# Kernel tuning notes

Hardware: AMD Instinct MI355X
Metric: run time of the kernel (lower is better)

Reference implementation:

```python
import jax, jax.numpy as jnp
import numpy as np

N_NODES = 100000
N_EDGES = 1250000
D_IN = 64
D_OUT = 64


def setup_inputs() -> dict:
    key = jax.random.key(0)
    k1, k2, k3, k4, k5 = jax.random.split(key, 5)
    x = jax.random.normal(k1, (N_NODES, D_IN), dtype=jnp.float32)
    edge_index = jax.random.randint(k2, (2, N_EDGES), 0, N_NODES, dtype=jnp.int64)
    # Linear weights stored torch-style as [out, in]
    w_neigh = jax.random.normal(k3, (D_OUT, D_IN), dtype=jnp.float32) / np.sqrt(D_IN)
    w_self = jax.random.normal(k4, (D_OUT, D_IN), dtype=jnp.float32) / np.sqrt(D_IN)
    b_self = jax.random.normal(k5, (D_OUT,), dtype=jnp.float32) * 0.01
    return {"x": x, "edge_index": edge_index, "w_neigh": w_neigh, "w_self": w_self, "b_self": b_self}


def reference(x, edge_index, w_neigh, w_self, b_self):
    num_nodes = x.shape[0]
    src, dst = edge_index[0], edge_index[1]
    # mean aggregation of neighbor features: scatter-add then divide by in-degree
    agg = jax.ops.segment_sum(x[src], dst, num_segments=num_nodes)  # [N, d]
    degree = jax.ops.segment_sum(jnp.ones_like(dst, dtype=x.dtype), dst, num_segments=num_nodes)
    degree = jnp.maximum(degree, 1.0)
    agg = agg / degree[:, None]
    return agg @ w_neigh.T + x @ w_self.T + b_self
```

## Files before the change

### kernel.cpp

```cpp
#include <hip/hip_runtime.h>

#define N_NODES 100000
#define N_EDGES 1250000
#define D 64
#define BSH 6
#define BNODES 64
#define NB 1563
#define WSW 68
#define G 512
#define CHUNK 2444
#define BIN_BLOCKS 128
#define BIN_CHUNK ((N_EDGES + BIN_BLOCKS - 1) / BIN_BLOCKS)

typedef unsigned int u32;
typedef short bf16x8 __attribute__((ext_vector_type(8)));
typedef float f32x4 __attribute__((ext_vector_type(4)));

__device__ __forceinline__ u32 pack_bf16(float lo, float hi) {
    u32 a = __float_as_uint(lo);
    u32 b = __float_as_uint(hi);
    a = (a + 0x7fffu + ((a >> 16) & 1u)) >> 16;
    b = (b + 0x7fffu + ((b >> 16) & 1u)) >> 16;
    return a | (b << 16);
}

__global__ void __launch_bounds__(256) k_wprep2(const float* __restrict__ wn,
                                                const float* __restrict__ wsf,
                                                u32* __restrict__ bfrag) {
    int i = blockIdx.x * 256 + threadIdx.x;
    if (i >= 4096) return;
    int t = i >> 9, h = (i >> 8) & 1, l = (i >> 2) & 63, q = i & 3;
    int k0 = h * 32 + (l >> 4) * 8 + 2 * q;
    int n = t * 16 + (l & 15);
    const float* w = (n < 64) ? &wn[(size_t)n * 64] : &wsf[(size_t)(n - 64) * 64];
    bfrag[i] = pack_bf16(w[k0], w[k0 + 1]);
}

__global__ void __launch_bounds__(256) k_hist(const int* __restrict__ ei,
                                              u32* __restrict__ ghist) {
    __shared__ u32 hist[NB];
    int tid = threadIdx.x;
    int g = blockIdx.x;
    int e0 = g * CHUNK, e1 = min(e0 + CHUNK, N_EDGES);
    for (int i = tid; i < NB; i += 256) hist[i] = 0;
    __syncthreads();
    const int4* dp = (const int4*)(ei + N_EDGES + e0);
    int nv = (e1 - e0) >> 2;
    for (int i = tid; i < nv; i += 256) {
        int4 d4 = dp[i];
        atomicAdd(&hist[d4.x >> BSH], 1u);
        atomicAdd(&hist[d4.y >> BSH], 1u);
        atomicAdd(&hist[d4.z >> BSH], 1u);
        atomicAdd(&hist[d4.w >> BSH], 1u);
    }
    __syncthreads();
    for (int i = tid; i < NB; i += 256)
        ghist[(size_t)i * G + g] = hist[i];
}

__global__ void __launch_bounds__(512) k_scanB(const u32* __restrict__ ghist,
                                               u32* __restrict__ gbase,
                                               u32* __restrict__ bcnt) {
    __shared__ u32 wt[8];
    int t = threadIdx.x;
    int b = blockIdx.x;
    int lane = t & 63, wv = t >> 6;
    u32 v = ghist[(size_t)b * G + t];
    u32 s = v;
#pragma unroll
    for (int off = 1; off < 64; off <<= 1) {
        u32 n = __shfl_up(s, off, 64);
        if (lane >= off) s += n;
    }
    if (lane == 63) wt[wv] = s;
    __syncthreads();
    u32 add = 0;
#pragma unroll
    for (int q = 0; q < 8; ++q) add += (q < wv) ? wt[q] : 0u;
    u32 incl = s + add;
    gbase[(size_t)b * G + t] = incl - v;
    if (t == G - 1) bcnt[b] = incl;
}

__global__ void __launch_bounds__(256) k_scat(const int* __restrict__ ei,
                                              const u32* __restrict__ gbase,
                                              u32* __restrict__ binned,
                                              int cap) {
    __shared__ u32 cur[NB];
    int tid = threadIdx.x;
    int g = blockIdx.x;
    int e0 = g * CHUNK, e1 = min(e0 + CHUNK, N_EDGES);
    for (int i = tid; i < NB; i += 256)
        cur[i] = gbase[(size_t)i * G + g];
    __syncthreads();
    const int4* sp = (const int4*)(ei + e0);
    const int4* dp = (const int4*)(ei + N_EDGES + e0);
    int nv = (e1 - e0) >> 2;
    for (int i = tid; i < nv; i += 256) {
        int4 s4 = sp[i];
        int4 d4 = dp[i];
        int ss[4] = {s4.x, s4.y, s4.z, s4.w};
        int dd[4] = {d4.x, d4.y, d4.z, d4.w};
#pragma unroll
        for (int u = 0; u < 4; ++u) {
            int b = dd[u] >> BSH;
            u32 loc = atomicAdd(&cur[b], 1u);
            if (loc < (u32)cap)
                binned[(size_t)b * cap + loc] = ((u32)ss[u] << BSH) | (u32)(dd[u] & (BNODES - 1));
        }
    }
}

__global__ void __launch_bounds__(256) k_mm(const float* __restrict__ x,
                                            const u32* __restrict__ bfrag,
                                            const float* __restrict__ bias,
                                            u32* __restrict__ y16,
                                            float* __restrict__ zout) {
    int tid = threadIdx.x;
    int w = tid >> 6, l = tid & 63;
    int lg = l >> 4, c = l & 15;
    int nodebase = blockIdx.x * 128 + w * 32;

    union FU { uint4 u; bf16x8 v; };

    bf16x8 af[2][2];
#pragma unroll
    for (int m = 0; m < 2; ++m) {
        int node = nodebase + m * 16 + c;
        if (node >= N_NODES) node = N_NODES - 1;
        const float4* xr = (const float4*)(x + (size_t)node * D);
#pragma unroll
        for (int h = 0; h < 2; ++h) {
            float4 p0 = xr[h * 8 + lg * 2];
            float4 p1 = xr[h * 8 + lg * 2 + 1];
            FU au;
            au.u.x = pack_bf16(p0.x, p0.y);
            au.u.y = pack_bf16(p0.z, p0.w);
            au.u.z = pack_bf16(p1.x, p1.y);
            au.u.w = pack_bf16(p1.z, p1.w);
            af[m][h] = au.v;
        }
    }

    f32x4 acc[2][8];
#pragma unroll
    for (int m = 0; m < 2; ++m) {
#pragma unroll
        for (int t = 0; t < 4; ++t) acc[m][t] = (f32x4){0.f, 0.f, 0.f, 0.f};
#pragma unroll
        for (int t = 4; t < 8; ++t) {
            float bb = bias[(t - 4) * 16 + c];
            acc[m][t] = (f32x4){bb, bb, bb, bb};
        }
    }

    const uint4* bp = (const uint4*)bfrag;
#pragma unroll
    for (int tc = 0; tc < 2; ++tc) {
        bf16x8 bf[4][2];
#pragma unroll
        for (int tt = 0; tt < 4; ++tt)
#pragma unroll
            for (int h = 0; h < 2; ++h) {
                FU bu;
                bu.u = bp[(((tc * 4 + tt) * 2 + h) * 64) + l];
                bf[tt][h] = bu.v;
            }
#pragma unroll
        for (int m = 0; m < 2; ++m)
#pragma unroll
            for (int tt = 0; tt < 4; ++tt) {
                int t = tc * 4 + tt;
                acc[m][t] = __builtin_amdgcn_mfma_f32_16x16x32_bf16(
                    af[m][0], bf[tt][0], acc[m][t], 0, 0, 0);
                acc[m][t] = __builtin_amdgcn_mfma_f32_16x16x32_bf16(
                    af[m][1], bf[tt][1], acc[m][t], 0, 0, 0);
            }
    }

#pragma unroll
    for (int m = 0; m < 2; ++m) {
        int rowbase = nodebase + m * 16 + lg * 4;
#pragma unroll
        for (int r = 0; r < 4; ++r) {
            int node = rowbase + r;
            bool ok = node < N_NODES;
#pragma unroll
            for (int t = 4; t < 8; ++t) {
                if (ok) zout[(size_t)node * D + (t - 4) * 16 + c] = acc[m][t][r];
            }
#pragma unroll
            for (int t = 0; t < 4; ++t) {
                float v = acc[m][t][r];
                float o = __shfl_xor(v, 1);
                if (ok && !(c & 1))
                    y16[(size_t)node * 32 + t * 8 + (c >> 1)] = pack_bf16(v, o);
            }
        }
    }
}

__global__ void __launch_bounds__(256) k_sort(u32* __restrict__ binned,
                                              const u32* __restrict__ bcnt,
                                              int cap,
                                              uint2* __restrict__ meta) {
    __shared__ u32 eh[1024];
    __shared__ u32 hist[BNODES];
    __shared__ u32 cur[BNODES];
    int tid = threadIdx.x;
    int b = blockIdx.x;
    int cnt = min((int)bcnt[b], cap);
    u32* seg = binned + (size_t)b * cap;

    if (tid < BNODES) hist[tid] = 0;
    __syncthreads();
    const uint4* segv = (const uint4*)seg;
    int nv = cnt >> 2;
    for (int i = tid; i < nv; i += 256) {
        uint4 w4 = segv[i];
        *(uint4*)&eh[4 * i] = w4;
        atomicAdd(&hist[w4.x & (BNODES - 1)], 1u);
        atomicAdd(&hist[w4.y & (BNODES - 1)], 1u);
        atomicAdd(&hist[w4.z & (BNODES - 1)], 1u);
        atomicAdd(&hist[w4.w & (BNODES - 1)], 1u);
    }
    for (int i = (cnt & ~3) + tid; i < cnt; i += 256) {
        u32 w = seg[i];
        eh[i] = w;
        atomicAdd(&hist[w & (BNODES - 1)], 1u);
    }
    __syncthreads();
    if (tid < BNODES) {
        u32 v = hist[tid];
        u32 s = v;
#pragma unroll
        for (int off = 1; off < 64; off <<= 1) {
            u32 n = __shfl_up(s, off, 64);
            if (tid >= off) s += n;
        }
        u32 excl = s - v;
        cur[tid] = excl;
        int node = (b << BSH) + tid;
        if (node < N_NODES)
            meta[node] = make_uint2((u32)((size_t)b * cap + excl), v);
    }
    __syncthreads();
    for (int i = tid; i < cnt; i += 256) {
        u32 w = eh[i];
        u32 p = atomicAdd(&cur[w & (BNODES - 1)], 1u);
        seg[p] = w >> BSH;
    }
}

__global__ void __launch_bounds__(256) k_gather_yz(const u32* __restrict__ y16,
                                                   const u32* __restrict__ binned,
                                                   const uint2* __restrict__ meta,
                                                   float* __restrict__ io) {
    int tid = blockIdx.x * 256 + threadIdx.x;
    int node = tid >> 6;
    if (node >= N_NODES) return;
    int lane = threadIdx.x & 63;
    int sub = lane >> 4;
    int pr = lane & 15;
    const uint2* yv = (const uint2*)y16;
    uint2 m = meta[node];
    u32 o0 = m.x, dg = m.y;

    u32 myidx = 0;
    if (lane < (int)dg) myidx = binned[o0 + lane];

    float a0 = 0.f, a1 = 0.f, a2 = 0.f, a3 = 0.f;
    u32 dmain = min(dg, 64u);
    for (u32 r = 0; r < dmain; r += 32) {
        uint2 w[8];
#pragma unroll
        for (int t = 0; t < 8; ++t) {
            u32 e = r + 4 * t + sub;
            u32 idx = (u32)__shfl((int)myidx, (int)(e & 63));
            w[t] = make_uint2(0u, 0u);
            if (e < dmain) w[t] = yv[(size_t)idx * 16 + pr];
        }
#pragma unroll
        for (int t = 0; t < 8; ++t) {
            if (r + 4u * (u32)t < dmain) {
                a0 += __uint_as_float(w[t].x << 16);
                a1 += __uint_as_float(w[t].x & 0xffff0000u);
                a2 += __uint_as_float(w[t].y << 16);
                a3 += __uint_as_float(w[t].y & 0xffff0000u);
            }
        }
    }
    for (u32 j = o0 + 64; j < o0 + dg; j += 16) {
#pragma unroll
        for (int t = 0; t < 4; ++t) {
            u32 ie = j + 4 * t + sub;
            if (ie < o0 + dg) {
                u32 idx = binned[ie];
                uint2 w = yv[(size_t)idx * 16 + pr];
                a0 += __uint_as_float(w.x << 16);
                a1 += __uint_as_float(w.x & 0xffff0000u);
                a2 += __uint_as_float(w.y << 16);
                a3 += __uint_as_float(w.y & 0xffff0000u);
            }
        }
    }

    a0 += __shfl_xor(a0, 16); a1 += __shfl_xor(a1, 16);
    a2 += __shfl_xor(a2, 16); a3 += __shfl_xor(a3, 16);
    a0 += __shfl_xor(a0, 32); a1 += __shfl_xor(a1, 32);
    a2 += __shfl_xor(a2, 32); a3 += __shfl_xor(a3, 32);
    if (sub == 0) {
        float inv = 1.0f / (float)max(dg, 1u);
        float4 z = *(const float4*)&io[(size_t)node * D + 4 * pr];
        *(float4*)&io[(size_t)node * D + 4 * pr] =
            make_float4(z.x + a0 * inv, z.y + a1 * inv, z.z + a2 * inv, z.w + a3 * inv);
    }
}

__global__ void __launch_bounds__(256) k_bin2(const int* __restrict__ ei,
                                              u32* __restrict__ bcnt,
                                              u32* __restrict__ binned,
                                              int cap) {
    __shared__ u32 hist[NB];
    __shared__ u32 rbase[NB];
    int tid = threadIdx.x;
    int e0 = blockIdx.x * BIN_CHUNK;
    int e1 = min(e0 + BIN_CHUNK, N_EDGES);
    const int* dstp = ei + N_EDGES;
    for (int i = tid; i < NB; i += 256) hist[i] = 0;
    __syncthreads();
    for (int e = e0 + tid; e < e1; e += 256)
        atomicAdd(&hist[dstp[e] >> BSH], 1u);
    __syncthreads();
    for (int i = tid; i < NB; i += 256) {
        u32 h = hist[i];
        rbase[i] = h ? atomicAdd(&bcnt[i], h) : 0u;
        hist[i] = 0;
    }
    __syncthreads();
    for (int e = e0 + tid; e < e1; e += 256) {
        int d = dstp[e];
        int s = ei[e];
        int b = d >> BSH;
        u32 loc = atomicAdd(&hist[b], 1u);
        u32 slot = rbase[b] + loc;
        if (slot < (u32)cap)
            binned[(size_t)b * cap + slot] = ((u32)s << BSH) | (u32)(d & (BNODES - 1));
    }
}

__global__ void __launch_bounds__(256) k_sort_fb(u32* __restrict__ binned,
                                                 const u32* __restrict__ bcnt,
                                                 int cap,
                                                 u32* __restrict__ offs,
                                                 u32* __restrict__ deg) {
    __shared__ u32 eh[1024];
    __shared__ u32 hist[BNODES];
    __shared__ u32 cur[BNODES];
    int tid = threadIdx.x;
    int b = blockIdx.x;
    int cnt = min((int)bcnt[b], cap);
    u32* seg = binned + (size_t)b * cap;
    if (tid < BNODES) hist[tid] = 0;
    __syncthreads();
    for (int i = tid; i < cnt; i += 256) {
        u32 w = seg[i];
        eh[i] = w;
        atomicAdd(&hist[w & (BNODES - 1)], 1u);
    }
    __syncthreads();
    if (tid < BNODES) {
        u32 v = hist[tid];
        u32 s = v;
#pragma unroll
        for (int off = 1; off < 64; off <<= 1) {
            u32 n = __shfl_up(s, off, 64);
            if (tid >= off) s += n;
        }
        u32 excl = s - v;
        cur[tid] = excl;
        int node = (b << BSH) + tid;
        if (node < N_NODES) {
            offs[node] = (u32)((size_t)b * cap + excl);
            deg[node] = v;
        }
    }
    __syncthreads();
    for (int i = tid; i < cnt; i += 256) {
        u32 w = eh[i];
        u32 p = atomicAdd(&cur[w & (BNODES - 1)], 1u);
        seg[p] = w >> BSH;
    }
}

__global__ void __launch_bounds__(256) k_gather32(const float* __restrict__ x,
                                                  const u32* __restrict__ binned,
                                                  const u32* __restrict__ offs,
                                                  const u32* __restrict__ deg,
                                                  float* __restrict__ agg) {
    int tid = blockIdx.x * 256 + threadIdx.x;
    int node = tid >> 6;
    int d = tid & 63;
    if (node >= N_NODES) return;
    u32 o0 = offs[node], dg = deg[node];
    u32 o1 = o0 + dg;
    float s = 0.f;
    u32 j = o0;
    for (; j + 8 <= o1; j += 8) {
        u32 e[8];
        float v[8];
#pragma unroll
        for (int t = 0; t < 8; ++t) e[t] = binned[j + t];
#pragma unroll
        for (int t = 0; t < 8; ++t) v[t] = x[(size_t)e[t] * D + d];
#pragma unroll
        for (int t = 0; t < 8; ++t) s += v[t];
    }
    for (; j < o1; ++j) s += x[(size_t)binned[j] * D + d];
    agg[(size_t)node * D + d] = s / (float)max(dg, 1u);
}

__global__ void __launch_bounds__(256) k_gemm_fb(const float* __restrict__ x,
                                                 const float* __restrict__ wn,
                                                 const float* __restrict__ wsf,
                                                 const float* __restrict__ bias,
                                                 float* __restrict__ io) {
    __shared__ float At[BNODES * WSW];
    __shared__ float Wt[128 * WSW];
    int tid = threadIdx.x;
    int base = blockIdx.x * 64;
    const float4* iop = (const float4*)io;
    const float4* xp  = (const float4*)x;
    for (int i = tid; i < 4096; i += 256) {
        int d = i >> 6, k = i & 63;
        Wt[k * WSW + d] = wn[i];
        Wt[(64 + k) * WSW + d] = wsf[i];
    }
    for (int i = tid; i < 1024; i += 256) {
        int r = i >> 4, q = i & 15;
        int node = base + r;
        float4 v = make_float4(0.f, 0.f, 0.f, 0.f);
        if (node < N_NODES) v = iop[(size_t)node * 16 + q];
        *(float4*)&At[r * WSW + q * 4] = v;
    }
    __syncthreads();
    int tn = tid >> 4, td = tid & 15;
    int n0 = tn * 4, d0 = td * 4;
    float4 b4 = *(const float4*)&bias[d0];
    float acc[4][4];
#pragma unroll
    for (int i = 0; i < 4; ++i) {
        acc[i][0] = b4.x; acc[i][1] = b4.y; acc[i][2] = b4.z; acc[i][3] = b4.w;
    }
#pragma unroll 8
    for (int kc = 0; kc < 16; ++kc) {
        float4 a[4], w[4];
#pragma unroll
        for (int i = 0; i < 4; ++i) a[i] = *(const float4*)&At[(n0 + i) * WSW + kc * 4];
#pragma unroll
        for (int t = 0; t < 4; ++t) w[t] = *(const float4*)&Wt[(kc * 4 + t) * WSW + d0];
#pragma unroll
        for (int i = 0; i < 4; ++i) {
            const float av[4] = {a[i].x, a[i].y, a[i].z, a[i].w};
#pragma unroll
            for (int t = 0; t < 4; ++t) {
                acc[i][0] += av[t] * w[t].x; acc[i][1] += av[t] * w[t].y;
                acc[i][2] += av[t] * w[t].z; acc[i][3] += av[t] * w[t].w;
            }
        }
    }
    __syncthreads();
    for (int i = tid; i < 1024; i += 256) {
        int r = i >> 4, q = i & 15;
        int node = base + r;
        float4 v = make_float4(0.f, 0.f, 0.f, 0.f);
        if (node < N_NODES) v = xp[(size_t)node * 16 + q];
        *(float4*)&At[r * WSW + q * 4] = v;
    }
    __syncthreads();
#pragma unroll 8
    for (int kc = 0; kc < 16; ++kc) {
        float4 a[4], w[4];
#pragma unroll
        for (int i = 0; i < 4; ++i) a[i] = *(const float4*)&At[(n0 + i) * WSW + kc * 4];
#pragma unroll
        for (int t = 0; t < 4; ++t) w[t] = *(const float4*)&Wt[(64 + kc * 4 + t) * WSW + d0];
#pragma unroll
        for (int i = 0; i < 4; ++i) {
            const float av[4] = {a[i].x, a[i].y, a[i].z, a[i].w};
#pragma unroll
            for (int t = 0; t < 4; ++t) {
                acc[i][0] += av[t] * w[t].x; acc[i][1] += av[t] * w[t].y;
                acc[i][2] += av[t] * w[t].z; acc[i][3] += av[t] * w[t].w;
            }
        }
    }
#pragma unroll
    for (int i = 0; i < 4; ++i) {
        int node = base + n0 + i;
        if (node < N_NODES) {
            *(float4*)&io[(size_t)node * D + d0] =
                make_float4(acc[i][0], acc[i][1], acc[i][2], acc[i][3]);
        }
    }
}

extern "C" void kernel_launch(void* const* d_in, const int* in_sizes, int n_in,
                              void* d_out, int out_size, void* d_ws, size_t ws_size,
                              hipStream_t stream) {
    const float* x = (const float*)d_in[0];
    const int* ei = (const int*)d_in[1];
    const float* wn = (const float*)d_in[2];
    const float* wsf = (const float*)d_in[3];
    const float* bias = (const float*)d_in[4];
    float* out = (float*)d_out;

    u32* metaw = (u32*)d_ws;
    u32* bcnt = metaw + 2 * N_NODES;
    u32* bfrag = bcnt + ((NB + 15) & ~15);
    u32* y16 = bfrag + 8192;
    const size_t Y16W = (size_t)N_NODES * (D / 2);
    u32* binned = y16 + Y16W;
    size_t fixed = 2 * (size_t)N_NODES + ((NB + 15) & ~15) + 8192;

    if (ws_size / 4 >= fixed + Y16W + (size_t)NB * 1024) {
        const int cap = 1024;
        u32* ghist = binned;
        u32* gbase = y16;
        k_wprep2<<<16, 256, 0, stream>>>(wn, wsf, bfrag);
        k_hist<<<G, 256, 0, stream>>>(ei, ghist);
        k_scanB<<<NB, 512, 0, stream>>>(ghist, gbase, bcnt);
        k_scat<<<G, 256, 0, stream>>>(ei, gbase, binned, cap);
        k_mm<<<(N_NODES + 127) / 128, 256, 0, stream>>>(x, bfrag, bias, y16, out);
        k_sort<<<NB, 256, 0, stream>>>(binned, bcnt, cap, (uint2*)metaw);
        k_gather_yz<<<(N_NODES * 64) / 256, 256, 0, stream>>>(y16, binned, (const uint2*)metaw, out);
    } else {
        u32* offs = metaw;
        u32* deg = offs + N_NODES;
        binned = bfrag;
        size_t avail = ws_size / 4 - (fixed - 8192);
        size_t capz = (avail / NB) & ~(size_t)3;
        int cap = (int)(capz < 1024 ? capz : 1024);
        hipMemsetAsync(bcnt, 0, ((NB + 15) & ~15) * sizeof(u32), stream);
        k_bin2<<<BIN_BLOCKS, 256, 0, stream>>>(ei, bcnt, binned, cap);
        k_sort_fb<<<NB, 256, 0, stream>>>(binned, bcnt, cap, offs, deg);
        k_gather32<<<(N_NODES * 64) / 256, 256, 0, stream>>>(x, binned, offs, deg, out);
        k_gemm_fb<<<(N_NODES + 63) / 64, 256, 0, stream>>>(x, wn, wsf, bias, out);
    }
}
```

Baseline: 100.3 us.

## Fuse weight prep into histogram and matmul into scatter kernel

Merges the weight-fragment prep kernel into the histogram kernel as an extra block, and merges the dense bf16 matmul into the edge scatter kernel via blockIdx dispatch. This cuts two kernel launches and lets the compute-bound matmul blocks run alongside the atomic-heavy scatter blocks. To avoid aliasing, ghist and gbase move to dedicated workspace regions, which raises the workspace requirement for the fast path. The merged kernel's LDS and register footprint is the maximum of the two roles, which may lower occupancy for the matmul blocks.

```diff
diff --git a/kernel.cpp b/kernel.cpp
--- a/kernel.cpp
+++ b/kernel.cpp
@@ -9,6 +9,7 @@
 #define WSW 68
 #define G 512
 #define CHUNK 2444
+#define MM_BLOCKS ((N_NODES + 127) / 128)
 #define BIN_BLOCKS 128
 #define BIN_CHUNK ((N_EDGES + BIN_BLOCKS - 1) / BIN_BLOCKS)
 
@@ -24,38 +25,39 @@
     return a | (b << 16);
 }
 
-__global__ void __launch_bounds__(256) k_wprep2(const float* __restrict__ wn,
-                                                const float* __restrict__ wsf,
-                                                u32* __restrict__ bfrag) {
-    int i = blockIdx.x * 256 + threadIdx.x;
-    if (i >= 4096) return;
-    int t = i >> 9, h = (i >> 8) & 1, l = (i >> 2) & 63, q = i & 3;
-    int k0 = h * 32 + (l >> 4) * 8 + 2 * q;
-    int n = t * 16 + (l & 15);
-    const float* w = (n < 64) ? &wn[(size_t)n * 64] : &wsf[(size_t)(n - 64) * 64];
-    bfrag[i] = pack_bf16(w[k0], w[k0 + 1]);
-}
-
-__global__ void __launch_bounds__(256) k_hist(const int* __restrict__ ei,
-                                              u32* __restrict__ ghist) {
+__global__ void __launch_bounds__(256) k_histw(const int* __restrict__ ei,
+                                               u32* __restrict__ ghist,
+                                               const float* __restrict__ wn,
+                                               const float* __restrict__ wsf,
+                                               u32* __restrict__ bfrag) {
     __shared__ u32 hist[NB];
     int tid = threadIdx.x;
-    int g = blockIdx.x;
-    int e0 = g * CHUNK, e1 = min(e0 + CHUNK, N_EDGES);
-    for (int i = tid; i < NB; i += 256) hist[i] = 0;
-    __syncthreads();
-    const int4* dp = (const int4*)(ei + N_EDGES + e0);
-    int nv = (e1 - e0) >> 2;
-    for (int i = tid; i < nv; i += 256) {
-        int4 d4 = dp[i];
-        atomicAdd(&hist[d4.x >> BSH], 1u);
-        atomicAdd(&hist[d4.y >> BSH], 1u);
-        atomicAdd(&hist[d4.z >> BSH], 1u);
-        atomicAdd(&hist[d4.w >> BSH], 1u);
-    }
-    __syncthreads();
-    for (int i = tid; i < NB; i += 256)
-        ghist[(size_t)i * G + g] = hist[i];
+    if (blockIdx.x < G) {
+        int g = blockIdx.x;
+        int e0 = g * CHUNK, e1 = min(e0 + CHUNK, N_EDGES);
+        for (int i = tid; i < NB; i += 256) hist[i] = 0;
+        __syncthreads();
+        const int4* dp = (const int4*)(ei + N_EDGES + e0);
+        int nv = (e1 - e0) >> 2;
+        for (int i = tid; i < nv; i += 256) {
+            int4 d4 = dp[i];
+            atomicAdd(&hist[d4.x >> BSH], 1u);
+            atomicAdd(&hist[d4.y >> BSH], 1u);
+            atomicAdd(&hist[d4.z >> BSH], 1u);
+            atomicAdd(&hist[d4.w >> BSH], 1u);
+        }
+        __syncthreads();
+        for (int i = tid; i < NB; i += 256)
+            ghist[(size_t)i * G + g] = hist[i];
+    } else {
+        for (int i = tid; i < 4096; i += 256) {
+            int t = i >> 9, h = (i >> 8) & 1, l = (i >> 2) & 63, q = i & 3;
+            int k0 = h * 32 + (l >> 4) * 8 + 2 * q;
+            int n = t * 16 + (l & 15);
+            const float* w = (n < 64) ? &wn[(size_t)n * 64] : &wsf[(size_t)(n - 64) * 64];
+            bfrag[i] = pack_bf16(w[k0], w[k0 + 1]);
+        }
+    }
 }
 
 __global__ void __launch_bounds__(512) k_scanB(const u32* __restrict__ ghist,
@@ -82,44 +84,45 @@
     if (t == G - 1) bcnt[b] = incl;
 }
 
-__global__ void __launch_bounds__(256) k_scat(const int* __restrict__ ei,
-                                              const u32* __restrict__ gbase,
-                                              u32* __restrict__ binned,
-                                              int cap) {
+__global__ void __launch_bounds__(256) k_scatmm(const int* __restrict__ ei,
+                                                const u32* __restrict__ gbase,
+                                                u32* __restrict__ binned,
+                                                int cap,
+                                                const float* __restrict__ x,
+                                                const u32* __restrict__ bfrag,
+                                                const float* __restrict__ bias,
+                                                u32* __restrict__ y16,
+                                                float* __restrict__ zout) {
     __shared__ u32 cur[NB];
     int tid = threadIdx.x;
-    int g = blockIdx.x;
-    int e0 = g * CHUNK, e1 = min(e0 + CHUNK, N_EDGES);
-    for (int i = tid; i < NB; i += 256)
-        cur[i] = gbase[(size_t)i * G + g];
-    __syncthreads();
-    const int4* sp = (const int4*)(ei + e0);
-    const int4* dp = (const int4*)(ei + N_EDGES + e0);
-    int nv = (e1 - e0) >> 2;
-    for (int i = tid; i < nv; i += 256) {
-        int4 s4 = sp[i];
-        int4 d4 = dp[i];
-        int ss[4] = {s4.x, s4.y, s4.z, s4.w};
-        int dd[4] = {d4.x, d4.y, d4.z, d4.w};
-#pragma unroll
-        for (int u = 0; u < 4; ++u) {
-            int b = dd[u] >> BSH;
-            u32 loc = atomicAdd(&cur[b], 1u);
-            if (loc < (u32)cap)
-                binned[(size_t)b * cap + loc] = ((u32)ss[u] << BSH) | (u32)(dd[u] & (BNODES - 1));
-        }
-    }
-}
-
-__global__ void __launch_bounds__(256) k_mm(const float* __restrict__ x,
-                                            const u32* __restrict__ bfrag,
-                                            const float* __restrict__ bias,
-                                            u32* __restrict__ y16,
-                                            float* __restrict__ zout) {
-    int tid = threadIdx.x;
+    if (blockIdx.x < G) {
+        int g = blockIdx.x;
+        int e0 = g * CHUNK, e1 = min(e0 + CHUNK, N_EDGES);
+        for (int i = tid; i < NB; i += 256)
+            cur[i] = gbase[(size_t)i * G + g];
+        __syncthreads();
+        const int4* sp = (const int4*)(ei + e0);
+        const int4* dp = (const int4*)(ei + N_EDGES + e0);
+        int nv = (e1 - e0) >> 2;
+        for (int i = tid; i < nv; i += 256) {
+            int4 s4 = sp[i];
+            int4 d4 = dp[i];
+            int ss[4] = {s4.x, s4.y, s4.z, s4.w};
+            int dd[4] = {d4.x, d4.y, d4.z, d4.w};
+#pragma unroll
+            for (int u = 0; u < 4; ++u) {
+                int b = dd[u] >> BSH;
+                u32 loc = atomicAdd(&cur[b], 1u);
+                if (loc < (u32)cap)
+                    binned[(size_t)b * cap + loc] = ((u32)ss[u] << BSH) | (u32)(dd[u] & (BNODES - 1));
+            }
+        }
+        return;
+    }
+
     int w = tid >> 6, l = tid & 63;
     int lg = l >> 4, c = l & 15;
-    int nodebase = blockIdx.x * 128 + w * 32;
+    int nodebase = (blockIdx.x - G) * 128 + w * 32;
 
     union FU { uint4 u; bf16x8 v; };
 
@@ -521,17 +524,17 @@
     u32* y16 = bfrag + 8192;
     const size_t Y16W = (size_t)N_NODES * (D / 2);
     u32* binned = y16 + Y16W;
+    u32* ghist = binned + (size_t)NB * 1024;
+    u32* gbase = ghist + (size_t)NB * G;
     size_t fixed = 2 * (size_t)N_NODES + ((NB + 15) & ~15) + 8192;
-
-    if (ws_size / 4 >= fixed + Y16W + (size_t)NB * 1024) {
+    size_t need = fixed + Y16W + (size_t)NB * 1024 + 2 * (size_t)NB * G;
+
+    if (ws_size / 4 >= need) {
         const int cap = 1024;
-        u32* ghist = binned;
-        u32* gbase = y16;
-        k_wprep2<<<16, 256, 0, stream>>>(wn, wsf, bfrag);
-        k_hist<<<G, 256, 0, stream>>>(ei, ghist);
+        k_histw<<<G + 1, 256, 0, stream>>>(ei, ghist, wn, wsf, bfrag);
         k_scanB<<<NB, 512, 0, stream>>>(ghist, gbase, bcnt);
-        k_scat<<<G, 256, 0, stream>>>(ei, gbase, binned, cap);
-        k_mm<<<(N_NODES + 127) / 128, 256, 0, stream>>>(x, bfrag, bias, y16, out);
+        k_scatmm<<<G + MM_BLOCKS, 256, 0, stream>>>(ei, gbase, binned, cap,
+                                                    x, bfrag, bias, y16, out);
         k_sort<<<NB, 256, 0, stream>>>(binned, bcnt, cap, (uint2*)metaw);
         k_gather_yz<<<(N_NODES * 64) / 256, 256, 0, stream>>>(y16, binned, (const uint2*)metaw, out);
     } else {
```

New measurement: 91.18 us. 9.1% less time.
